# Kernel tuning notes

Measured on AMD Instinct MI355X. Metric: run time of the kernel, lower is better.

The kernel has to match this reference:

```python
import jax, jax.numpy as jnp
import numpy as np

EPS = 1e-05


def setup_inputs() -> dict:
    key = jax.random.key(0)
    k1, k2, k3, k4 = jax.random.split(key, 4)
    B, N, L, J = 1, 256, 192, 32
    n_feat_out = 128
    d2 = J * J  # 1024
    x_down = jax.random.normal(k1, (B, N, L, J), dtype=jnp.float32)
    x_down_w = jax.random.normal(k2, (B, N, L, J), dtype=jnp.float32)
    a_2 = jnp.ones((d2,), dtype=jnp.float32)
    b_2 = jnp.zeros((d2,), dtype=jnp.float32)
    # nn.Linear default init: U(-1/sqrt(fan_in), 1/sqrt(fan_in))
    bound = 1.0 / np.sqrt(d2)
    W = jax.random.uniform(k3, (d2, n_feat_out), dtype=jnp.float32, minval=-bound, maxval=bound)
    b = jax.random.uniform(k4, (n_feat_out,), dtype=jnp.float32, minval=-bound, maxval=bound)
    return {"x_down": x_down, "x_down_w": x_down_w, "a_2": a_2, "b_2": b_2, "W": W, "b": b}


def reference(x_down, x_down_w, a_2, b_2, W, b):
    B, N, L, J = x_down.shape
    # outer-product contraction over MSA dim: (B,L,L,J,J)
    pair = jnp.einsum('bnij,bnlm->biljm', x_down, x_down_w)
    pair = pair.reshape(B, L, L, J * J)
    # LayerNorm over last dim (biased variance, matching torch unbiased=False)
    mean = pair.mean(axis=-1, keepdims=True)
    var = pair.var(axis=-1, keepdims=True)
    pair = a_2 * (pair - mean) / jnp.sqrt(var + EPS) + b_2
    # Linear projection J^2 -> n_feat_out
    return pair @ W + b
```

## Files before the change

### kernel.cpp

```cpp
#include <hip/hip_runtime.h>
#include <hip/hip_bf16.h>
#include <stdint.h>

#define NN   256
#define LL   192
#define MDIM 6144
#define D2   1024
#define FF   128

typedef __bf16 bf16x8 __attribute__((ext_vector_type(8)));
typedef float  f32x4  __attribute__((ext_vector_type(4)));

#define MFMA16(a, b, c) __builtin_amdgcn_mfma_f32_16x16x32_bf16(a, b, c, 0, 0, 0)

__device__ __forceinline__ void gload_lds16(const void* g, void* l) {
  __builtin_amdgcn_global_load_lds(
      (__attribute__((address_space(1))) void*)(g),
      (__attribute__((address_space(3))) void*)(l),
      16, 0, 0);
}

static __device__ __forceinline__ unsigned short bf16_bits(float v) {
  __bf16 h = (__bf16)v;
  return __builtin_bit_cast(unsigned short, h);
}

__global__ __launch_bounds__(256)
void prep_all(const float* __restrict__ x1, const float* __restrict__ x2,
              const float* __restrict__ W, const float* __restrict__ a2,
              const float* __restrict__ b2, const float* __restrict__ bias,
              __bf16* __restrict__ At, __bf16* __restrict__ Bt,
              __bf16* __restrict__ WB, float* __restrict__ S,
              float* __restrict__ T) {
  __shared__ float tile[32][33];
  const int b = blockIdx.x;
  const int t = threadIdx.x;
  if (b < 3072) {
    const float* src = (b < 1536) ? x1 : x2;
    __bf16* dst = (b < 1536) ? At : Bt;
    const int bb = (b < 1536) ? b : b - 1536;
    const int m0 = (bb % 192) * 32;
    const int k0 = (bb / 192) * 32;
    {
      const int kr = t >> 3, mc = (t & 7) * 4;
      const float4 v = *(const float4*)&src[(size_t)(k0 + kr) * MDIM + m0 + mc];
      tile[kr][mc + 0] = v.x;
      tile[kr][mc + 1] = v.y;
      tile[kr][mc + 2] = v.z;
      tile[kr][mc + 3] = v.w;
    }
    __syncthreads();
    {
      const int mr = t >> 3, kc = (t & 7) * 4;
      ushort4 u;
      u.x = bf16_bits(tile[kc + 0][mr]);
      u.y = bf16_bits(tile[kc + 1][mr]);
      u.z = bf16_bits(tile[kc + 2][mr]);
      u.w = bf16_bits(tile[kc + 3][mr]);
      *(ushort4*)&dst[(size_t)(m0 + mr) * NN + k0 + kc] = u;
    }
  } else {
    const int f = b - 3072;
    float s = 0.f, tt = 0.f;
#pragma unroll
    for (int it = 0; it < 4; ++it) {
      const int k = t + it * 256;
      const float wv = W[(size_t)k * FF + f];
      const __bf16 wa = (__bf16)(a2[k] * wv);
      WB[(size_t)(k >> 5) * 4096 + f * 32 + ((k >> 3) & 3) * 8 + (k & 7)] = wa;
      s += (float)wa;
      tt += b2[k] * wv;
    }
#pragma unroll
    for (int off = 32; off; off >>= 1) {
      s += __shfl_xor(s, off);
      tt += __shfl_xor(tt, off);
    }
    const int wv_ = t >> 6, ln = t & 63;
    if (ln == 0) { tile[0][wv_] = s; tile[1][wv_] = tt; }
    __syncthreads();
    if (t == 0) {
      S[f] = tile[0][0] + tile[0][1] + tile[0][2] + tile[0][3];
      T[f] = tile[1][0] + tile[1][1] + tile[1][2] + tile[1][3] + bias[f];
    }
  }
}

__global__ __launch_bounds__(256, 4)
void fused7(const __bf16* __restrict__ At, const __bf16* __restrict__ Bt,
            const __bf16* __restrict__ WB, const float* __restrict__ S,
            const float* __restrict__ T, float* __restrict__ out) {
  __shared__ uint8_t lds[32768];
  __shared__ float mean_s[16], rstd_s[16];

  const int tid = threadIdx.x;
  const int w = tid >> 6;
  const int lane = tid & 63;
  const int q = lane >> 4;
  const int c = lane & 15;

  const int b = blockIdx.x;
  const int xcd = b & 7;
  const int s_ = b >> 3;
  const int bx = (xcd >> 1) * 12 + (s_ % 12);
  const int by = (xcd & 1) * 24 + (s_ / 12);
  const int m0 = bx * 128, n0 = by * 128;

  uint8_t* As = lds;
  uint8_t* Bs = lds + 16384;

  const int l8 = lane & 7;
  const int r8 = lane >> 3;
  const int gsw = l8 ^ r8;

  f32x4 acc[4][4];
#pragma unroll
  for (int i = 0; i < 4; ++i)
#pragma unroll
    for (int j = 0; j < 4; ++j)
      acc[i][j] = (f32x4){0.f, 0.f, 0.f, 0.f};

  const int mbase = (w & 1) * 64;
  const int nbase = (w >> 1) * 64;

  {
    const __bf16* gA = At + (size_t)(m0 + w * 8 + r8) * NN + gsw * 8;
    const __bf16* gB = Bt + (size_t)(n0 + w * 8 + r8) * NN + gsw * 8;
    uint8_t* dst = As + (w * 8) * 128;
#pragma unroll 1
    for (int kb = 0; kb < 4; ++kb) {
      __syncthreads();
#pragma unroll
      for (int s4 = 0; s4 < 4; ++s4) {
        gload_lds16(gA + (size_t)s4 * 32 * NN, dst + s4 * 4096);
        gload_lds16(gB + (size_t)s4 * 32 * NN, dst + 16384 + s4 * 4096);
      }
      __syncthreads();
#pragma unroll
      for (int ks = 0; ks < 2; ++ks) {
        const int slot = ((ks * 4 + q) ^ (lane & 7)) * 16;
        bf16x8 a[4];
#pragma unroll
        for (int t4 = 0; t4 < 4; ++t4)
          a[t4] = *(const bf16x8*)(As + (mbase + t4 * 16 + c) * 128 + slot);
#pragma unroll
        for (int tj = 0; tj < 4; ++tj) {
          const bf16x8 bfr =
              *(const bf16x8*)(Bs + (nbase + tj * 16 + c) * 128 + slot);
#pragma unroll
          for (int ti = 0; ti < 4; ++ti)
            acc[ti][tj] = MFMA16(a[ti], bfr, acc[ti][tj]);
        }
      }
      gA += 64;
      gB += 64;
    }
  }

  const int fb = w * 32;
  const __bf16* wb0 = WB + (fb + c) * 32 + q * 8;
  const __bf16* wb1 = WB + (fb + 16 + c) * 32 + q * 8;
  bf16x8 pb0[2], pb1[2];
#pragma unroll
  for (int p = 0; p < 2; ++p) {
    pb0[p] = *(const bf16x8*)(wb0 + p * 4096);
    pb1[p] = *(const bf16x8*)(wb1 + p * 4096);
  }

  __syncthreads();

  const int i_hi = w & 1, l_hi = w >> 1;
#pragma unroll
  for (int ab = 0; ab < 2; ++ab) {
#pragma unroll
    for (int cb = 0; cb < 2; ++cb) {
      float s1 = 0.f, s2 = 0.f;
#pragma unroll
      for (int dti = 0; dti < 2; ++dti)
#pragma unroll
        for (int dtj = 0; dtj < 2; ++dtj)
#pragma unroll
          for (int reg = 0; reg < 4; ++reg) {
            const float v = acc[ab * 2 + dti][cb * 2 + dtj][reg];
            s1 += v; s2 += v * v;
          }
#pragma unroll
      for (int off = 32; off; off >>= 1) {
        s1 += __shfl_xor(s1, off);
        s2 += __shfl_xor(s2, off);
      }
      const float mean = s1 * (1.0f / 1024.0f);
      const float var = s2 * (1.0f / 1024.0f) - mean * mean;
      const float rstd = rsqrtf(var + 1e-5f);
      const int r = (i_hi * 2 + ab) * 4 + (l_hi * 2 + cb);
      if (lane == 0) { mean_s[r] = mean; rstd_s[r] = rstd; }
      const int r7 = r & 7;
#pragma unroll
      for (int dti = 0; dti < 2; ++dti)
#pragma unroll
        for (int dtj = 0; dtj < 2; ++dtj)
#pragma unroll
          for (int rp = 0; rp < 4; rp += 2) {
            const float x = acc[ab * 2 + dti][cb * 2 + dtj][rp];
            const float y = acc[ab * 2 + dti][cb * 2 + dtj][rp + 1];
            const float send = (c & 1) ? x : y;
            const float recv = __shfl_xor(send, 1);
            const float vlo = (c & 1) ? recv : x;
            const float vhi = (c & 1) ? y : recv;
            const int reg_w = (c & 1) ? rp + 1 : rp;
            const int j = dti * 16 + q * 4 + reg_w;
            const int mm0 = dtj * 16 + (c & ~1);
            const int k = j * 32 + mm0;
            const int g = k >> 3;
            const int G = g ^ (g >> 4) ^ r7;
            const uint32_t dw =
                ((uint32_t)bf16_bits(vhi) << 16) | (uint32_t)bf16_bits(vlo);
            *(uint32_t*)(lds + r * 2048 + G * 16 + (mm0 & 7) * 2) = dw;
          }
    }
  }

  __syncthreads();

  f32x4 acc2[2];
  acc2[0] = (f32x4){0.f, 0.f, 0.f, 0.f};
  acc2[1] = (f32x4){0.f, 0.f, 0.f, 0.f};
  const int c7 = c & 7;
#pragma unroll
  for (int kstep = 0; kstep < 32; ++kstep) {
    const int g = kstep * 4 + q;
    const int G = g ^ (g >> 4) ^ c7;
    const bf16x8 av = *(const bf16x8*)(lds + c * 2048 + G * 16);
    acc2[0] = MFMA16(av, pb0[kstep & 1], acc2[0]);
    acc2[1] = MFMA16(av, pb1[kstep & 1], acc2[1]);
    if (kstep < 30) {
      pb0[kstep & 1] = *(const bf16x8*)(wb0 + (kstep + 2) * 4096);
      pb1[kstep & 1] = *(const bf16x8*)(wb1 + (kstep + 2) * 4096);
    }
  }

  const float S0 = S[fb + c], T0 = T[fb + c];
  const float S1 = S[fb + 16 + c], T1 = T[fb + 16 + c];
#pragma unroll
  for (int reg = 0; reg < 4; ++reg) {
    const int r = q * 4 + reg;
    const float mean = mean_s[r], rstd = rstd_s[r];
    const int i = bx * 4 + (r >> 2);
    const int l = by * 4 + (r & 3);
    const size_t base = ((size_t)i * LL + l) * FF;
    out[base + fb + c]      = rstd * (acc2[0][reg] - mean * S0) + T0;
    out[base + fb + 16 + c] = rstd * (acc2[1][reg] - mean * S1) + T1;
  }
}

extern "C" void kernel_launch(void* const* d_in, const int* in_sizes, int n_in,
                              void* d_out, int out_size, void* d_ws, size_t ws_size,
                              hipStream_t stream) {
  const float* x_down   = (const float*)d_in[0];
  const float* x_down_w = (const float*)d_in[1];
  const float* a2       = (const float*)d_in[2];
  const float* b2       = (const float*)d_in[3];
  const float* W        = (const float*)d_in[4];
  const float* bias     = (const float*)d_in[5];
  float* out = (float*)d_out;

  uint8_t* ws = (uint8_t*)d_ws;
  __bf16* At  = (__bf16*)(ws);
  __bf16* Bt  = (__bf16*)(ws + 3145728);
  __bf16* WB  = (__bf16*)(ws + 6291456);
  float*  S   = (float*)(ws + 6553600);
  float*  T   = (float*)(ws + 6554112);

  prep_all<<<dim3(3200), dim3(256), 0, stream>>>(x_down, x_down_w, W, a2, b2,
                                                 bias, At, Bt, WB, S, T);
  fused7<<<dim3(2304), dim3(256), 0, stream>>>(At, Bt, WB, S, T, out);
}
```

Measured before the change: 138.9 us.

## Widen fused GEMM tile to 128x256 with 512-thread blocks sharing W fragments

Doubles the N-extent of each block's outer-product tile to 256 columns and uses 8 waves per block, halving the grid. In the projection stage each wave now owns 16 output features across 32 pair rows, so every W fragment loaded feeds two MFMAs. W prefetch is deepened to 8 stages and issued after the barrier. The aim is to cut global traffic for W and A per output, at the cost of doubling LDS to 64KB per block, which may lower occupancy.

```diff
diff --git a/kernel.cpp b/kernel.cpp
--- a/kernel.cpp
+++ b/kernel.cpp
@@ -86,12 +86,12 @@
   }
 }
 
-__global__ __launch_bounds__(256, 4)
-void fused7(const __bf16* __restrict__ At, const __bf16* __restrict__ Bt,
-            const __bf16* __restrict__ WB, const float* __restrict__ S,
-            const float* __restrict__ T, float* __restrict__ out) {
-  __shared__ uint8_t lds[32768];
-  __shared__ float mean_s[16], rstd_s[16];
+__global__ __launch_bounds__(512, 4)
+void fused10(const __bf16* __restrict__ At, const __bf16* __restrict__ Bt,
+             const __bf16* __restrict__ WB, const float* __restrict__ S,
+             const float* __restrict__ T, float* __restrict__ out) {
+  __shared__ uint8_t lds[65536];
+  __shared__ float mean_s[32], rstd_s[32];
 
   const int tid = threadIdx.x;
   const int w = tid >> 6;
@@ -103,8 +103,8 @@
   const int xcd = b & 7;
   const int s_ = b >> 3;
   const int bx = (xcd >> 1) * 12 + (s_ % 12);
-  const int by = (xcd & 1) * 24 + (s_ / 12);
-  const int m0 = bx * 128, n0 = by * 128;
+  const int by = (xcd & 1) * 12 + (s_ / 12);
+  const int m0 = bx * 128, n0 = by * 256;
 
   uint8_t* As = lds;
   uint8_t* Bs = lds + 16384;
@@ -124,17 +124,17 @@
   const int nbase = (w >> 1) * 64;
 
   {
-    const __bf16* gA = At + (size_t)(m0 + w * 8 + r8) * NN + gsw * 8;
-    const __bf16* gB = Bt + (size_t)(n0 + w * 8 + r8) * NN + gsw * 8;
-    uint8_t* dst = As + (w * 8) * 128;
+    const __bf16* gA = At + (size_t)(m0 + w * 16 + r8) * NN + gsw * 8;
+    const __bf16* gB = Bt + (size_t)(n0 + w * 32 + r8) * NN + gsw * 8;
 #pragma unroll 1
     for (int kb = 0; kb < 4; ++kb) {
       __syncthreads();
 #pragma unroll
-      for (int s4 = 0; s4 < 4; ++s4) {
-        gload_lds16(gA + (size_t)s4 * 32 * NN, dst + s4 * 4096);
-        gload_lds16(gB + (size_t)s4 * 32 * NN, dst + 16384 + s4 * 4096);
-      }
+      for (int j = 0; j < 2; ++j)
+        gload_lds16(gA + (size_t)j * 8 * NN, As + (w * 16 + j * 8) * 128);
+#pragma unroll
+      for (int j = 0; j < 4; ++j)
+        gload_lds16(gB + (size_t)j * 8 * NN, Bs + (w * 32 + j * 8) * 128);
       __syncthreads();
 #pragma unroll
       for (int ks = 0; ks < 2; ++ks) {
@@ -157,15 +157,11 @@
     }
   }
 
-  const int fb = w * 32;
-  const __bf16* wb0 = WB + (fb + c) * 32 + q * 8;
-  const __bf16* wb1 = WB + (fb + 16 + c) * 32 + q * 8;
-  bf16x8 pb0[2], pb1[2];
-#pragma unroll
-  for (int p = 0; p < 2; ++p) {
-    pb0[p] = *(const bf16x8*)(wb0 + p * 4096);
-    pb1[p] = *(const bf16x8*)(wb1 + p * 4096);
-  }
+  const int fs = w * 16;
+  const __bf16* wbp = WB + (fs + c) * 32 + q * 8;
+  bf16x8 pb[8];
+  pb[0] = *(const bf16x8*)(wbp);
+  pb[1] = *(const bf16x8*)(wbp + 4096);
 
   __syncthreads();
 
@@ -192,7 +188,7 @@
       const float mean = s1 * (1.0f / 1024.0f);
       const float var = s2 * (1.0f / 1024.0f) - mean * mean;
       const float rstd = rsqrtf(var + 1e-5f);
-      const int r = (i_hi * 2 + ab) * 4 + (l_hi * 2 + cb);
+      const int r = (i_hi * 2 + ab) * 8 + l_hi * 2 + cb;
       if (lane == 0) { mean_s[r] = mean; rstd_s[r] = rstd; }
       const int r7 = r & 7;
 #pragma unroll
@@ -221,6 +217,11 @@
   }
 
   __syncthreads();
+  __builtin_amdgcn_sched_barrier(0);
+
+#pragma unroll
+  for (int p = 2; p < 8; ++p)
+    pb[p] = *(const bf16x8*)(wbp + p * 4096);
 
   f32x4 acc2[2];
   acc2[0] = (f32x4){0.f, 0.f, 0.f, 0.f};
@@ -230,26 +231,33 @@
   for (int kstep = 0; kstep < 32; ++kstep) {
     const int g = kstep * 4 + q;
     const int G = g ^ (g >> 4) ^ c7;
-    const bf16x8 av = *(const bf16x8*)(lds + c * 2048 + G * 16);
-    acc2[0] = MFMA16(av, pb0[kstep & 1], acc2[0]);
-    acc2[1] = MFMA16(av, pb1[kstep & 1], acc2[1]);
-    if (kstep < 30) {
-      pb0[kstep & 1] = *(const bf16x8*)(wb0 + (kstep + 2) * 4096);
-      pb1[kstep & 1] = *(const bf16x8*)(wb1 + (kstep + 2) * 4096);
-    }
-  }
-
-  const float S0 = S[fb + c], T0 = T[fb + c];
-  const float S1 = S[fb + 16 + c], T1 = T[fb + 16 + c];
+    const bf16x8 a0 = *(const bf16x8*)(lds + c * 2048 + G * 16);
+    const bf16x8 a1 = *(const bf16x8*)(lds + (16 + c) * 2048 + G * 16);
+    acc2[0] = MFMA16(a0, pb[kstep & 7], acc2[0]);
+    acc2[1] = MFMA16(a1, pb[kstep & 7], acc2[1]);
+    if (kstep < 24)
+      pb[kstep & 7] = *(const bf16x8*)(wbp + (kstep + 8) * 4096);
+  }
+
+  const float S0 = S[fs + c], T0 = T[fs + c];
 #pragma unroll
   for (int reg = 0; reg < 4; ++reg) {
-    const int r = q * 4 + reg;
-    const float mean = mean_s[r], rstd = rstd_s[r];
-    const int i = bx * 4 + (r >> 2);
-    const int l = by * 4 + (r & 3);
-    const size_t base = ((size_t)i * LL + l) * FF;
-    out[base + fb + c]      = rstd * (acc2[0][reg] - mean * S0) + T0;
-    out[base + fb + 16 + c] = rstd * (acc2[1][reg] - mean * S1) + T1;
+    const int r0 = q * 4 + reg;
+    const int r1 = 16 + r0;
+    {
+      const float mean = mean_s[r0], rstd = rstd_s[r0];
+      const int i = bx * 4 + (r0 >> 3);
+      const int l = by * 8 + (r0 & 7);
+      out[((size_t)i * LL + l) * FF + fs + c] =
+          rstd * (acc2[0][reg] - mean * S0) + T0;
+    }
+    {
+      const float mean = mean_s[r1], rstd = rstd_s[r1];
+      const int i = bx * 4 + (r1 >> 3);
+      const int l = by * 8 + (r1 & 7);
+      out[((size_t)i * LL + l) * FF + fs + c] =
+          rstd * (acc2[1][reg] - mean * S0) + T0;
+    }
   }
 }
 
@@ -273,5 +281,5 @@
 
   prep_all<<<dim3(3200), dim3(256), 0, stream>>>(x_down, x_down_w, W, a2, b2,
                                                  bias, At, Bt, WB, S, T);
-  fused7<<<dim3(2304), dim3(256), 0, stream>>>(At, Bt, WB, S, T, out);
-}
+  fused10<<<dim3(1152), dim3(512), 0, stream>>>(At, Bt, WB, S, T, out);
+}
```

Result: faster. 126.4 us (-9.0%).
